# Kernel optimization log

Measured on AMD Instinct MI355X. Metric: run time of the kernel, lower is better.

## Reference

```python
import jax, jax.numpy as jnp
import numpy as np

HEADS = 8

def setup_inputs() -> dict:
    key = jax.random.key(0)
    ks = jax.random.split(key, 5)
    B, C, H, W = 2, 256, 64, 64
    dim = C
    x = jax.random.normal(ks[0], (B, C, H, W), dtype=jnp.float32)
    # Linear weights stored as [in, out] so y = x @ W + b
    w_qkv = jax.random.normal(ks[1], (dim, 3 * dim), dtype=jnp.float32) * (dim ** -0.5)
    b_qkv = jax.random.normal(ks[2], (3 * dim,), dtype=jnp.float32) * 0.02
    w_out = jax.random.normal(ks[3], (dim, dim), dtype=jnp.float32) * (dim ** -0.5)
    b_out = jax.random.normal(ks[4], (dim,), dtype=jnp.float32) * 0.02
    return {"x": x, "w_qkv": w_qkv, "b_qkv": b_qkv, "w_out": w_out, "b_out": b_out}

def reference(x, w_qkv, b_qkv, w_out, b_out):
    B, C, H, W = x.shape
    h = HEADS
    d = C // h
    scale = d ** -0.5
    # [B, C, H, W] -> [B, N, C]
    tokens = x.reshape(B, C, H * W).transpose(0, 2, 1)
    qkv = tokens @ w_qkv + b_qkv  # [B, N, 3C]
    q, k, v = jnp.split(qkv, 3, axis=-1)
    def to_heads(t):
        Bn, N, _ = t.shape
        return t.reshape(Bn, N, h, d).transpose(0, 2, 1, 3)  # [B, h, N, d]
    q, k, v = map(to_heads, (q, k, v))
    dots = jnp.einsum('bhnd,bhmd->bhnm', q, k) * scale  # [B, h, N, N]
    attn = jax.nn.softmax(dots, axis=-1)
    out = jnp.einsum('bhnm,bhmd->bhnd', attn, v)  # [B, h, N, d]
    out = out.transpose(0, 2, 1, 3).reshape(B, H * W, C)  # [B, N, C]
    out = out @ w_out + b_out
    return out.transpose(0, 2, 1).reshape(B, C, H, W)
```

## Files before the change

kernel.cpp:

```cpp
#include <hip/hip_runtime.h>

typedef __attribute__((ext_vector_type(8))) short s16x8;
typedef __attribute__((ext_vector_type(4))) float f32x4;
typedef __attribute__((ext_vector_type(16))) float f32x16;
typedef __attribute__((ext_vector_type(2))) unsigned u32x2;
typedef __attribute__((ext_vector_type(4))) unsigned u32x4;

#define MFMA32(a, b, c) __builtin_amdgcn_mfma_f32_16x16x32_bf16((a), (b), (c), 0, 0, 0)

#if __has_builtin(__builtin_amdgcn_mfma_f32_32x32x16_bf16)
#define MFMA3216(a, b, c) __builtin_amdgcn_mfma_f32_32x32x16_bf16((a), (b), (c), 0, 0, 0)
#else
#define MFMA3216(a, b, c) (c)
#endif

#if __has_builtin(__builtin_amdgcn_exp2f)
#define EXP2F(x) __builtin_amdgcn_exp2f(x)
#else
#define EXP2F(x) __exp2f(x)
#endif

#if __has_builtin(__builtin_amdgcn_rcpf)
#define RCPF(x) __builtin_amdgcn_rcpf(x)
#else
#define RCPF(x) (1.0f / (x))
#endif

#define SL2E 0.25507313f

__device__ __forceinline__ unsigned pkrne(float a, float b) {
  unsigned ua = __builtin_bit_cast(unsigned, a);
  unsigned ub = __builtin_bit_cast(unsigned, b);
  ua += 0x7FFFu + ((ua >> 16) & 1u);
  ub += 0x7FFFu + ((ub >> 16) & 1u);
  return __builtin_amdgcn_perm(ub, ua, 0x07060302u);
}

__device__ __forceinline__ unsigned pktrunc(float a, float b) {
  return __builtin_amdgcn_perm(__builtin_bit_cast(unsigned, b),
                               __builtin_bit_cast(unsigned, a), 0x07060302u);
}

__device__ __forceinline__ unsigned short bfr(float f) {
  unsigned u = __builtin_bit_cast(unsigned, f);
  u += 0x7FFFu + ((u >> 16) & 1u);
  return (unsigned short)(u >> 16);
}

__device__ __forceinline__ float bflo(unsigned u) {
  return __builtin_bit_cast(float, u << 16);
}
__device__ __forceinline__ float bfhi(unsigned u) {
  return __builtin_bit_cast(float, u & 0xFFFF0000u);
}

__device__ __forceinline__ u32x2 plswap(unsigned a, unsigned b) {
#if __has_builtin(__builtin_amdgcn_permlane32_swap)
  return __builtin_amdgcn_permlane32_swap(a, b, false, false);
#else
  unsigned sa = (unsigned)__shfl_xor((int)a, 32, 64);
  unsigned sb = (unsigned)__shfl_xor((int)b, 32, 64);
  bool hi = (threadIdx.x & 63) >= 32;
  u32x2 r;
  r.x = hi ? sb : a;
  r.y = hi ? b : sa;
  return r;
#endif
}

__global__ __launch_bounds__(256) void prep_kernel(
    const float* __restrict__ x, const float* __restrict__ wqkv,
    const float* __restrict__ wout, ushort* __restrict__ xbf,
    ushort* __restrict__ wT, ushort* __restrict__ woT) {
  const int t = threadIdx.x;
  const int sub = t & 15, grp = t >> 4;
  const int id = blockIdx.x;
  const float* src;
  ushort* dst;
  int src_ld, k0, n0;
  float sc = 1.f;
  if (id < 512) {
    int mt = id & 63, kt = (id >> 6) & 3, b = id >> 8;
    src = x + (size_t)b * 256 * 4096;
    src_ld = 4096;
    dst = xbf + (size_t)b * 4096 * 256;
    k0 = kt * 64;
    n0 = mt * 64;
  } else if (id < 560) {
    int r = id - 512, nt = r % 12, kt = r / 12;
    src = wqkv;
    src_ld = 768;
    dst = wT;
    k0 = kt * 64;
    n0 = nt * 64;
    if (n0 < 256) sc = SL2E;
  } else {
    int r = id - 560, nt = r & 3, kt = r >> 2;
    src = wout;
    src_ld = 256;
    dst = woT;
    k0 = kt * 64;
    n0 = nt * 64;
  }
  const int k = k0 + grp * 4;
  const int n = n0 + sub * 4;
  unsigned d0[4], d1[4];
#pragma unroll
  for (int i = 0; i < 4; ++i) {
    float4 v = *(const float4*)(src + (size_t)(k + i) * src_ld + n);
    d0[i] = pkrne(v.x * sc, v.y * sc);
    d1[i] = pkrne(v.z * sc, v.w * sc);
  }
  u32x2 r0 = {__builtin_amdgcn_perm(d0[1], d0[0], 0x05040100u),
              __builtin_amdgcn_perm(d0[3], d0[2], 0x05040100u)};
  u32x2 r1 = {__builtin_amdgcn_perm(d0[1], d0[0], 0x07060302u),
              __builtin_amdgcn_perm(d0[3], d0[2], 0x07060302u)};
  u32x2 r2 = {__builtin_amdgcn_perm(d1[1], d1[0], 0x05040100u),
              __builtin_amdgcn_perm(d1[3], d1[2], 0x05040100u)};
  u32x2 r3 = {__builtin_amdgcn_perm(d1[1], d1[0], 0x07060302u),
              __builtin_amdgcn_perm(d1[3], d1[2], 0x07060302u)};
  *(u32x2*)(dst + (size_t)(n + 0) * 256 + k) = r0;
  *(u32x2*)(dst + (size_t)(n + 1) * 256 + k) = r1;
  *(u32x2*)(dst + (size_t)(n + 2) * 256 + k) = r2;
  *(u32x2*)(dst + (size_t)(n + 3) * 256 + k) = r3;
}

__global__ __launch_bounds__(256) void qkv_kernel(
    const ushort* __restrict__ xbf, const ushort* __restrict__ wT,
    const float* __restrict__ bq, ushort* __restrict__ QG,
    ushort* __restrict__ KG, ushort* __restrict__ VtG) {
  __shared__ __align__(16) ushort Wl[64][40];
  __shared__ __align__(16) ushort Xl[128][40];
  const int t0 = blockIdx.x * 128;
  const int n0 = blockIdx.y * 64;
  const int t = threadIdx.x;
  const int wid = t >> 6, lane = t & 63;
  const int wy = wid >> 1, wx = wid & 1;
  const int quad = lane >> 4, l16 = lane & 15;
  f32x4 acc[2][4] = {};
  const int wr = t >> 2, wsg = t & 3;
  for (int k0 = 0; k0 < 256; k0 += 32) {
    __syncthreads();
    *(uint4*)&Wl[wr][wsg * 8] =
        *(const uint4*)(wT + (size_t)(n0 + wr) * 256 + k0 + wsg * 8);
#pragma unroll
    for (int i = 0; i < 2; ++i) {
      int fid = t + 256 * i, row = fid >> 2, seg = fid & 3;
      *(uint4*)&Xl[row][seg * 8] =
          *(const uint4*)(xbf + (size_t)(t0 + row) * 256 + k0 + seg * 8);
    }
    __syncthreads();
    s16x8 wf[2], xf[4];
#pragma unroll
    for (int i = 0; i < 2; ++i)
      wf[i] = *(const s16x8*)&Wl[32 * wy + 16 * i + l16][quad * 8];
#pragma unroll
    for (int j = 0; j < 4; ++j)
      xf[j] = *(const s16x8*)&Xl[64 * wx + 16 * j + l16][quad * 8];
#pragma unroll
    for (int i = 0; i < 2; ++i)
#pragma unroll
      for (int j = 0; j < 4; ++j) acc[i][j] = MFMA32(wf[i], xf[j], acc[i][j]);
  }
  if (n0 < 256) {
#pragma unroll
    for (int i = 0; i < 2; ++i) {
      int nb = n0 + 32 * wy + 16 * i + 4 * quad;
      float4 b4 = *(const float4*)(bq + nb);
      float bx0 = b4.x * SL2E, bx1 = b4.y * SL2E, bx2 = b4.z * SL2E,
            bx3 = b4.w * SL2E;
      int h = ((nb & 255) >> 5);
      int dd0 = nb & 31;
#pragma unroll
      for (int j = 0; j < 4; ++j) {
        int tok = t0 + 64 * wx + 16 * j + l16;
        int b = tok >> 12, tokn = tok & 4095;
        u32x2 pk = {pkrne(acc[i][j][0] + bx0, acc[i][j][1] + bx1),
                    pkrne(acc[i][j][2] + bx2, acc[i][j][3] + bx3)};
        *(u32x2*)(QG + ((size_t)(b * 8 + h) * 4096 + tokn) * 32 + dd0) = pk;
      }
    }
  } else if (n0 < 512) {
#pragma unroll
    for (int i = 0; i < 2; ++i) {
      int nb = n0 + 32 * wy + 16 * i + 4 * quad;
      float4 b4 = *(const float4*)(bq + nb);
      float bx0 = b4.x, bx1 = b4.y, bx2 = b4.z, bx3 = b4.w;
      int h = ((nb & 255) >> 5);
      size_t fo = (size_t)i * 512 + (quad >> 1) * 256 + (quad & 1) * 4;
#pragma unroll
      for (int j = 0; j < 4; ++j) {
        int tok = t0 + 64 * wx + 16 * j + l16;
        int b = tok >> 12, tokn = tok & 4095;
        int tl = tokn >> 6, ss = (tokn >> 5) & 1, l5 = tokn & 31;
        u32x2 pk = {pkrne(acc[i][j][0] + bx0, acc[i][j][1] + bx1),
                    pkrne(acc[i][j][2] + bx2, acc[i][j][3] + bx3)};
        *(u32x2*)(KG + (size_t)(b * 8 + h) * 131072 + (size_t)tl * 2048 +
                  ss * 1024 + l5 * 8 + fo) = pk;
      }
    }
  } else {
#pragma unroll
    for (int i = 0; i < 2; ++i) {
      int nb = n0 + 32 * wy + 16 * i + 4 * quad;
      float4 b4 = *(const float4*)(bq + nb);
      float bb[4] = {b4.x, b4.y, b4.z, b4.w};
#pragma unroll
      for (int r = 0; r < 4; ++r) {
        int nn = nb + r - 512;
        int h = nn >> 5, d = nn & 31;
#pragma unroll
        for (int j = 0; j < 4; ++j) {
          int tok = t0 + 64 * wx + 16 * j + l16;
          int b = tok >> 12, tokn = tok & 4095;
          int tl = tokn >> 6, ss = (tokn >> 5) & 1;
          int hV = (tokn >> 4) & 1, hii = (tokn >> 3) & 1, e = tokn & 7;
          VtG[(size_t)(b * 8 + h) * 131072 + (size_t)tl * 2048 + ss * 1024 +
              hV * 512 + hii * 256 + d * 8 + e] = bfr(acc[i][j][r] + bb[r]);
        }
      }
    }
  }
}

__global__ __launch_bounds__(256, 4) void attn_split(
    const ushort* __restrict__ QG, const ushort* __restrict__ KG,
    const ushort* __restrict__ VtG, ushort* __restrict__ OF0,
    ushort* __restrict__ OFb, float* __restrict__ LF) {
  const int id = blockIdx.x;
  const int bh = (id & 7) * 2 + ((id >> 3) & 1);
  const int q0 = ((id >> 4) & 31) * 128;
  const int sp = id >> 9;
  const int kt0 = sp * 32;
  const int niter = 32;
  const int t = threadIdx.x;
  const int wid = t >> 6, lane = t & 63;
  const int l5 = lane & 31, hi = lane >> 5;
  const ushort* qp = QG + (size_t)bh * 4096 * 32;
  const ushort* kgp = KG + (size_t)bh * 131072 + (size_t)kt0 * 2048;
  const ushort* vgp = VtG + (size_t)bh * 131072 + (size_t)kt0 * 2048;
  const int qw = q0 + 32 * wid;
  const ushort* qrow = qp + (size_t)(qw + l5) * 32 + hi * 8;
  const s16x8 qf0 = *(const s16x8*)(qrow);
  const s16x8 qf1 = *(const s16x8*)(qrow + 16);
  f32x16 o = {};
  f32x16 o_l = {};
  const s16x8 ones8 = {(short)0x3F80, (short)0x3F80, (short)0x3F80,
                       (short)0x3F80, (short)0x3F80, (short)0x3F80,
                       (short)0x3F80, (short)0x3F80};
  const int lo8 = lane * 8;
  for (int i = 0; i < niter; ++i) {
    const ushort* kt = kgp + (size_t)i * 2048;
    const ushort* vt = vgp + (size_t)i * 2048;
    s16x8 k00 = *(const s16x8*)(kt + lo8);
    s16x8 k01 = *(const s16x8*)(kt + 512 + lo8);
    s16x8 v00 = *(const s16x8*)(vt + lo8);
    s16x8 v01 = *(const s16x8*)(vt + 512 + lo8);
    s16x8 k10 = *(const s16x8*)(kt + 1024 + lo8);
    s16x8 k11 = *(const s16x8*)(kt + 1536 + lo8);
    s16x8 v10 = *(const s16x8*)(vt + 1024 + lo8);
    s16x8 v11 = *(const s16x8*)(vt + 1536 + lo8);
#pragma unroll
    for (int s = 0; s < 2; ++s) {
      const s16x8 ka0 = s ? k10 : k00;
      const s16x8 ka1 = s ? k11 : k01;
      const s16x8 va0 = s ? v10 : v00;
      const s16x8 va1 = s ? v11 : v01;
      f32x16 S = {};
      S = MFMA3216(ka0, qf0, S);
      S = MFMA3216(ka1, qf1, S);
      unsigned w8[8];
#pragma unroll
      for (int ii = 0; ii < 8; ++ii)
        w8[ii] = pktrunc(EXP2F(S[2 * ii]), EXP2F(S[2 * ii + 1]));
      u32x2 sw0 = plswap(w8[0], w8[2]);
      u32x2 sw1 = plswap(w8[1], w8[3]);
      u32x2 sw2 = plswap(w8[4], w8[6]);
      u32x2 sw3 = plswap(w8[5], w8[7]);
      u32x4 pa0 = {sw0.x, sw1.x, sw0.y, sw1.y};
      u32x4 pa1 = {sw2.x, sw3.x, sw2.y, sw3.y};
      const s16x8 pA0 = __builtin_bit_cast(s16x8, pa0);
      const s16x8 pA1 = __builtin_bit_cast(s16x8, pa1);
      o = MFMA3216(pA0, va0, o);
      o = MFMA3216(pA1, va1, o);
      o_l = MFMA3216(pA0, ones8, o_l);
      o_l = MFMA3216(pA1, ones8, o_l);
    }
  }
  ushort* OFs = (sp == 0) ? OF0 : OFb;
  float* LFs = LF + (size_t)sp * 65536;
#pragma unroll
  for (int r = 0; r < 16; ++r) {
    int q = qw + (r & 3) + 8 * (r >> 2) + 4 * hi;
    OFs[((size_t)bh * 4096 + q) * 32 + l5] = bfr(o[r]);
  }
  float lval = o_l[0];
#pragma unroll
  for (int r = 1; r < 16; ++r) lval = (l5 == r) ? o_l[r] : lval;
  if (l5 < 16)
    LFs[(size_t)bh * 4096 + qw + (l5 & 3) + 8 * (l5 >> 2) + 4 * hi] = lval;
}

__global__ __launch_bounds__(256) void proj_split(
    const ushort* __restrict__ OF0, const ushort* __restrict__ OFb,
    const float* __restrict__ LF, const ushort* __restrict__ woT,
    const float* __restrict__ bo, float* __restrict__ out) {
  __shared__ __align__(16) ushort Wl[64][40];
  __shared__ __align__(16) ushort Xl[128][40];
  const int t0 = blockIdx.x * 128;
  const int c0 = blockIdx.y * 64;
  const int t = threadIdx.x;
  const int wid = t >> 6, lane = t & 63;
  const int wy = wid >> 1, wx = wid & 1;
  const int quad = lane >> 4, l16 = lane & 15;
  f32x4 acc[2][4] = {};
  const int wr = t >> 2, wsg = t & 3;
  const int c8 = (t & 7) * 4;
  for (int k0 = 0; k0 < 256; k0 += 32) {
    __syncthreads();
    *(uint4*)&Wl[wr][wsg * 8] =
        *(const uint4*)(woT + (size_t)(c0 + wr) * 256 + k0 + wsg * 8);
    const int hh = k0 >> 5;
#pragma unroll
    for (int p = 0; p < 4; ++p) {
      int row = 32 * p + (t >> 3);
      int tok = t0 + row, bb = tok >> 12, tokn = tok & 4095;
      size_t ro = (size_t)(bb * 8 + hh) * 4096 + tokn;
      size_t oi = ro * 32 + c8;
      uint2 a0 = *(const uint2*)(OF0 + oi);
      uint2 a1 = *(const uint2*)(OFb + oi);
      float l = LF[ro] + LF[65536 + ro];
      float inv = RCPF(l);
      f32x4 s;
      s[0] = bflo(a0.x) + bflo(a1.x);
      s[1] = bfhi(a0.x) + bfhi(a1.x);
      s[2] = bflo(a0.y) + bflo(a1.y);
      s[3] = bfhi(a0.y) + bfhi(a1.y);
      s *= inv;
      u32x2 pk = {pkrne(s[0], s[1]), pkrne(s[2], s[3])};
      *(u32x2*)&Xl[row][c8] = pk;
    }
    __syncthreads();
    s16x8 wf[2], xf[4];
#pragma unroll
    for (int i = 0; i < 2; ++i)
      wf[i] = *(const s16x8*)&Wl[32 * wy + 16 * i + l16][quad * 8];
#pragma unroll
    for (int j = 0; j < 4; ++j)
      xf[j] = *(const s16x8*)&Xl[64 * wx + 16 * j + l16][quad * 8];
#pragma unroll
    for (int i = 0; i < 2; ++i)
#pragma unroll
      for (int j = 0; j < 4; ++j) acc[i][j] = MFMA32(wf[i], xf[j], acc[i][j]);
  }
#pragma unroll
  for (int i = 0; i < 2; ++i) {
    int cb = c0 + 32 * wy + 16 * i + 4 * quad;
    float4 b4 = *(const float4*)(bo + cb);
    float bb[4] = {b4.x, b4.y, b4.z, b4.w};
#pragma unroll
    for (int j = 0; j < 4; ++j) {
      int tok = t0 + 64 * wx + 16 * j + l16;
      int b = tok >> 12, tokn = tok & 4095;
#pragma unroll
      for (int r = 0; r < 4; ++r)
        out[((size_t)(b * 256 + cb + r)) * 4096 + tokn] = acc[i][j][r] + bb[r];
    }
  }
}

extern "C" void kernel_launch(void* const* d_in, const int* in_sizes, int n_in,
                              void* d_out, int out_size, void* d_ws, size_t ws_size,
                              hipStream_t stream) {
  (void)in_sizes; (void)n_in; (void)out_size; (void)ws_size;
  const float* x = (const float*)d_in[0];
  const float* wq = (const float*)d_in[1];
  const float* bq = (const float*)d_in[2];
  const float* wo = (const float*)d_in[3];
  const float* bo = (const float*)d_in[4];
  float* out = (float*)d_out;
  ushort* ws = (ushort*)d_ws;
  ushort* xbf = ws;
  ushort* OF0 = ws;
  ushort* QG  = ws + 2097152;
  ushort* KG  = ws + 4194304;
  ushort* VtG = ws + 6291456;
  ushort* wT  = ws + 8388608;
  ushort* woT = ws + 8585216;
  ushort* OFb = ws + 8650752;
  float* LF = (float*)(ws + 12845056);
  prep_kernel<<<576, 256, 0, stream>>>(x, wq, wo, xbf, wT, woT);
  qkv_kernel<<<dim3(64, 12), 256, 0, stream>>>(xbf, wT, bq, QG, KG, VtG);
  attn_split<<<1024, 256, 0, stream>>>(QG, KG, VtG, OF0, OFb, LF);
  proj_split<<<dim3(64, 4), 256, 0, stream>>>(OF0, OFb, LF, woT, bo, out);
}
```

Baseline: 143.4 us.

## Stage K/V tiles through triple-buffered LDS with async loads and software-pipelined softmax

The attention kernel now copies K and V tiles into a three-deep shared-memory ring using direct global-to-LDS loads, replacing the per-wave global reads. The score MFMAs for one half-tile are interleaved with the softmax and PV step of the previous half-tile, so memory latency and exp work can overlap with matrix math. The K/V tiles are shared across the four waves of a block, with one barrier per iteration. Separately, the output projection tile is halved to 64 tokens, which doubles the grid for better CU occupancy at the cost of more redundant weight loads.

```diff
diff --git a/kernel.cpp b/kernel.cpp
--- a/kernel.cpp
+++ b/kernel.cpp
@@ -65,6 +65,19 @@
   r.x = hi ? sb : a;
   r.y = hi ? b : sa;
   return r;
+#endif
+}
+
+__device__ __forceinline__ void stage16(const ushort* g, ushort* l, int lane) {
+#if __has_builtin(__builtin_amdgcn_global_load_lds)
+  __builtin_amdgcn_global_load_lds(
+      (__attribute__((address_space(1))) unsigned int*)(unsigned long long)(
+          const void*)g,
+      (__attribute__((address_space(3))) unsigned int*)(unsigned)(
+          unsigned long long)(const void*)l,
+      16, 0, 0);
+#else
+  *(uint4*)(l + lane * 8) = *(const uint4*)g;
 #endif
 }
 
@@ -223,10 +236,41 @@
   }
 }
 
+struct AttnAcc {
+  f32x16 o;
+  f32x16 o_l;
+};
+
+__device__ __forceinline__ void softpv(const f32x16& S, const ushort* vhalf,
+                                       int lane, f32x16& o, f32x16& o_l) {
+  const s16x8 ones8 = {(short)0x3F80, (short)0x3F80, (short)0x3F80,
+                       (short)0x3F80, (short)0x3F80, (short)0x3F80,
+                       (short)0x3F80, (short)0x3F80};
+  unsigned w8[8];
+#pragma unroll
+  for (int ii = 0; ii < 8; ++ii)
+    w8[ii] = pktrunc(EXP2F(S[2 * ii]), EXP2F(S[2 * ii + 1]));
+  u32x2 sw0 = plswap(w8[0], w8[2]);
+  u32x2 sw1 = plswap(w8[1], w8[3]);
+  u32x2 sw2 = plswap(w8[4], w8[6]);
+  u32x2 sw3 = plswap(w8[5], w8[7]);
+  u32x4 pa0 = {sw0.x, sw1.x, sw0.y, sw1.y};
+  u32x4 pa1 = {sw2.x, sw3.x, sw2.y, sw3.y};
+  const s16x8 pA0 = __builtin_bit_cast(s16x8, pa0);
+  const s16x8 pA1 = __builtin_bit_cast(s16x8, pa1);
+  const s16x8 va0 = *(const s16x8*)(vhalf + lane * 8);
+  const s16x8 va1 = *(const s16x8*)(vhalf + 512 + lane * 8);
+  o = MFMA3216(pA0, va0, o);
+  o = MFMA3216(pA1, va1, o);
+  o_l = MFMA3216(pA0, ones8, o_l);
+  o_l = MFMA3216(pA1, ones8, o_l);
+}
+
 __global__ __launch_bounds__(256, 4) void attn_split(
     const ushort* __restrict__ QG, const ushort* __restrict__ KG,
     const ushort* __restrict__ VtG, ushort* __restrict__ OF0,
     ushort* __restrict__ OFb, float* __restrict__ LF) {
+  __shared__ __align__(64) ushort KVs[3][4096];
   const int id = blockIdx.x;
   const int bh = (id & 7) * 2 + ((id >> 3) & 1);
   const int q0 = ((id >> 4) & 31) * 128;
@@ -243,50 +287,46 @@
   const ushort* qrow = qp + (size_t)(qw + l5) * 32 + hi * 8;
   const s16x8 qf0 = *(const s16x8*)(qrow);
   const s16x8 qf1 = *(const s16x8*)(qrow + 16);
+  const int kdst = wid * 512;
+  const ushort* kpre = kgp + kdst + lane * 8;
+  const ushort* vpre = vgp + kdst + lane * 8;
+  stage16(kpre, &KVs[0][kdst], lane);
+  stage16(vpre, &KVs[0][2048 + kdst], lane);
+  kpre += 2048;
+  vpre += 2048;
+  __syncthreads();
   f32x16 o = {};
   f32x16 o_l = {};
-  const s16x8 ones8 = {(short)0x3F80, (short)0x3F80, (short)0x3F80,
-                       (short)0x3F80, (short)0x3F80, (short)0x3F80,
-                       (short)0x3F80, (short)0x3F80};
+  f32x16 S1p = {};
+  int b = 0, bm1 = 2, bp1 = 1;
   const int lo8 = lane * 8;
   for (int i = 0; i < niter; ++i) {
-    const ushort* kt = kgp + (size_t)i * 2048;
-    const ushort* vt = vgp + (size_t)i * 2048;
-    s16x8 k00 = *(const s16x8*)(kt + lo8);
-    s16x8 k01 = *(const s16x8*)(kt + 512 + lo8);
-    s16x8 v00 = *(const s16x8*)(vt + lo8);
-    s16x8 v01 = *(const s16x8*)(vt + 512 + lo8);
-    s16x8 k10 = *(const s16x8*)(kt + 1024 + lo8);
-    s16x8 k11 = *(const s16x8*)(kt + 1536 + lo8);
-    s16x8 v10 = *(const s16x8*)(vt + 1024 + lo8);
-    s16x8 v11 = *(const s16x8*)(vt + 1536 + lo8);
-#pragma unroll
-    for (int s = 0; s < 2; ++s) {
-      const s16x8 ka0 = s ? k10 : k00;
-      const s16x8 ka1 = s ? k11 : k01;
-      const s16x8 va0 = s ? v10 : v00;
-      const s16x8 va1 = s ? v11 : v01;
-      f32x16 S = {};
-      S = MFMA3216(ka0, qf0, S);
-      S = MFMA3216(ka1, qf1, S);
-      unsigned w8[8];
-#pragma unroll
-      for (int ii = 0; ii < 8; ++ii)
-        w8[ii] = pktrunc(EXP2F(S[2 * ii]), EXP2F(S[2 * ii + 1]));
-      u32x2 sw0 = plswap(w8[0], w8[2]);
-      u32x2 sw1 = plswap(w8[1], w8[3]);
-      u32x2 sw2 = plswap(w8[4], w8[6]);
-      u32x2 sw3 = plswap(w8[5], w8[7]);
-      u32x4 pa0 = {sw0.x, sw1.x, sw0.y, sw1.y};
-      u32x4 pa1 = {sw2.x, sw3.x, sw2.y, sw3.y};
-      const s16x8 pA0 = __builtin_bit_cast(s16x8, pa0);
-      const s16x8 pA1 = __builtin_bit_cast(s16x8, pa1);
-      o = MFMA3216(pA0, va0, o);
-      o = MFMA3216(pA1, va1, o);
-      o_l = MFMA3216(pA0, ones8, o_l);
-      o_l = MFMA3216(pA1, ones8, o_l);
-    }
-  }
+    if (i + 1 < niter) {
+      stage16(kpre, &KVs[bp1][kdst], lane);
+      stage16(vpre, &KVs[bp1][2048 + kdst], lane);
+      kpre += 2048;
+      vpre += 2048;
+    }
+    const ushort* kb = &KVs[b][0];
+    const s16x8 ka00 = *(const s16x8*)(kb + lo8);
+    const s16x8 ka01 = *(const s16x8*)(kb + 512 + lo8);
+    f32x16 S0 = {};
+    S0 = MFMA3216(ka00, qf0, S0);
+    S0 = MFMA3216(ka01, qf1, S0);
+    if (i > 0) softpv(S1p, &KVs[bm1][2048 + 1024], lane, o, o_l);
+    const s16x8 ka10 = *(const s16x8*)(kb + 1024 + lo8);
+    const s16x8 ka11 = *(const s16x8*)(kb + 1536 + lo8);
+    f32x16 S1 = {};
+    S1 = MFMA3216(ka10, qf0, S1);
+    S1 = MFMA3216(ka11, qf1, S1);
+    softpv(S0, &KVs[b][2048], lane, o, o_l);
+    S1p = S1;
+    __syncthreads();
+    bm1 = b;
+    b = bp1;
+    bp1 = (bp1 + 1 == 3) ? 0 : bp1 + 1;
+  }
+  softpv(S1p, &KVs[bm1][2048 + 1024], lane, o, o_l);
   ushort* OFs = (sp == 0) ? OF0 : OFb;
   float* LFs = LF + (size_t)sp * 65536;
 #pragma unroll
@@ -306,14 +346,14 @@
     const float* __restrict__ LF, const ushort* __restrict__ woT,
     const float* __restrict__ bo, float* __restrict__ out) {
   __shared__ __align__(16) ushort Wl[64][40];
-  __shared__ __align__(16) ushort Xl[128][40];
-  const int t0 = blockIdx.x * 128;
+  __shared__ __align__(16) ushort Xl[64][40];
+  const int t0 = blockIdx.x * 64;
   const int c0 = blockIdx.y * 64;
   const int t = threadIdx.x;
   const int wid = t >> 6, lane = t & 63;
   const int wy = wid >> 1, wx = wid & 1;
   const int quad = lane >> 4, l16 = lane & 15;
-  f32x4 acc[2][4] = {};
+  f32x4 acc[2][2] = {};
   const int wr = t >> 2, wsg = t & 3;
   const int c8 = (t & 7) * 4;
   for (int k0 = 0; k0 < 256; k0 += 32) {
@@ -322,7 +362,7 @@
         *(const uint4*)(woT + (size_t)(c0 + wr) * 256 + k0 + wsg * 8);
     const int hh = k0 >> 5;
 #pragma unroll
-    for (int p = 0; p < 4; ++p) {
+    for (int p = 0; p < 2; ++p) {
       int row = 32 * p + (t >> 3);
       int tok = t0 + row, bb = tok >> 12, tokn = tok & 4095;
       size_t ro = (size_t)(bb * 8 + hh) * 4096 + tokn;
@@ -341,17 +381,17 @@
       *(u32x2*)&Xl[row][c8] = pk;
     }
     __syncthreads();
-    s16x8 wf[2], xf[4];
+    s16x8 wf[2], xf[2];
 #pragma unroll
     for (int i = 0; i < 2; ++i)
       wf[i] = *(const s16x8*)&Wl[32 * wy + 16 * i + l16][quad * 8];
 #pragma unroll
-    for (int j = 0; j < 4; ++j)
-      xf[j] = *(const s16x8*)&Xl[64 * wx + 16 * j + l16][quad * 8];
+    for (int j = 0; j < 2; ++j)
+      xf[j] = *(const s16x8*)&Xl[32 * wx + 16 * j + l16][quad * 8];
 #pragma unroll
     for (int i = 0; i < 2; ++i)
 #pragma unroll
-      for (int j = 0; j < 4; ++j) acc[i][j] = MFMA32(wf[i], xf[j], acc[i][j]);
+      for (int j = 0; j < 2; ++j) acc[i][j] = MFMA32(wf[i], xf[j], acc[i][j]);
   }
 #pragma unroll
   for (int i = 0; i < 2; ++i) {
@@ -359,8 +399,8 @@
     float4 b4 = *(const float4*)(bo + cb);
     float bb[4] = {b4.x, b4.y, b4.z, b4.w};
 #pragma unroll
-    for (int j = 0; j < 4; ++j) {
-      int tok = t0 + 64 * wx + 16 * j + l16;
+    for (int j = 0; j < 2; ++j) {
+      int tok = t0 + 32 * wx + 16 * j + l16;
       int b = tok >> 12, tokn = tok & 4095;
 #pragma unroll
       for (int r = 0; r < 4; ++r)
@@ -392,5 +432,5 @@
   prep_kernel<<<576, 256, 0, stream>>>(x, wq, wo, xbf, wT, woT);
   qkv_kernel<<<dim3(64, 12), 256, 0, stream>>>(xbf, wT, bq, QG, KG, VtG);
   attn_split<<<1024, 256, 0, stream>>>(QG, KG, VtG, OF0, OFb, LF);
-  proj_split<<<dim3(64, 4), 256, 0, stream>>>(OF0, OFb, LF, woT, bo, out);
-}
+  proj_split<<<dim3(128, 4), 256, 0, stream>>>(OF0, OFb, LF, woT, bo, out);
+}
```

Result: faster. 136.6 us (-4.7%).

## Split attention keys three ways, software-pipeline K/V loads, shrink projection tiles

Applied to the files above, without the earlier changes.

The attention kernel now splits the 64 key tiles across three partitions instead of two, giving 1536 blocks, with the occupancy hint lowered from 4 to 3. Its inner loop double-buffers K/V register loads so the next tile's loads overlap the current tile's MFMAs. The projection kernel sums three partial outputs and normalizers and uses 64-token tiles, launching twice as many blocks. The aim is better GPU fill and latency hiding, at the cost of more partial-result traffic and register pressure.

```diff
diff --git a/kernel.cpp b/kernel.cpp
--- a/kernel.cpp
+++ b/kernel.cpp
@@ -223,7 +223,48 @@
   }
 }
 
-__global__ __launch_bounds__(256, 4) void attn_split(
+__device__ __forceinline__ void softpv(const f32x16& S, s16x8 va0, s16x8 va1,
+                                       f32x16& o, f32x16& o_l) {
+  const s16x8 ones8 = {(short)0x3F80, (short)0x3F80, (short)0x3F80,
+                       (short)0x3F80, (short)0x3F80, (short)0x3F80,
+                       (short)0x3F80, (short)0x3F80};
+  unsigned w8[8];
+#pragma unroll
+  for (int ii = 0; ii < 8; ++ii)
+    w8[ii] = pktrunc(EXP2F(S[2 * ii]), EXP2F(S[2 * ii + 1]));
+  u32x2 sw0 = plswap(w8[0], w8[2]);
+  u32x2 sw1 = plswap(w8[1], w8[3]);
+  u32x2 sw2 = plswap(w8[4], w8[6]);
+  u32x2 sw3 = plswap(w8[5], w8[7]);
+  u32x4 pa0 = {sw0.x, sw1.x, sw0.y, sw1.y};
+  u32x4 pa1 = {sw2.x, sw3.x, sw2.y, sw3.y};
+  const s16x8 pA0 = __builtin_bit_cast(s16x8, pa0);
+  const s16x8 pA1 = __builtin_bit_cast(s16x8, pa1);
+  o = MFMA3216(pA0, va0, o);
+  o = MFMA3216(pA1, va1, o);
+  o_l = MFMA3216(pA0, ones8, o_l);
+  o_l = MFMA3216(pA1, ones8, o_l);
+}
+
+#define LDT(F0, F1, F2, F3, P)            \
+  {                                       \
+    F0 = *(const s16x8*)((P));            \
+    F1 = *(const s16x8*)((P) + 512);      \
+    F2 = *(const s16x8*)((P) + 1024);     \
+    F3 = *(const s16x8*)((P) + 1536);     \
+  }
+
+#define TILE(K0, K1, K2, K3, V0, V1, V2, V3)   \
+  {                                            \
+    f32x16 S0 = MFMA3216(K0, qf0, fz);         \
+    S0 = MFMA3216(K1, qf1, S0);                \
+    softpv(S0, V0, V1, o, o_l);                \
+    f32x16 S1 = MFMA3216(K2, qf0, fz);         \
+    S1 = MFMA3216(K3, qf1, S1);                \
+    softpv(S1, V2, V3, o, o_l);                \
+  }
+
+__global__ __launch_bounds__(256, 3) void attn_split(
     const ushort* __restrict__ QG, const ushort* __restrict__ KG,
     const ushort* __restrict__ VtG, ushort* __restrict__ OF0,
     ushort* __restrict__ OFb, float* __restrict__ LF) {
@@ -231,63 +272,47 @@
   const int bh = (id & 7) * 2 + ((id >> 3) & 1);
   const int q0 = ((id >> 4) & 31) * 128;
   const int sp = id >> 9;
-  const int kt0 = sp * 32;
-  const int niter = 32;
+  const int kt0 = (sp * 64 + 2) / 3;
+  const int niter = ((sp + 1) * 64 + 2) / 3 - kt0;
   const int t = threadIdx.x;
   const int wid = t >> 6, lane = t & 63;
   const int l5 = lane & 31, hi = lane >> 5;
   const ushort* qp = QG + (size_t)bh * 4096 * 32;
-  const ushort* kgp = KG + (size_t)bh * 131072 + (size_t)kt0 * 2048;
-  const ushort* vgp = VtG + (size_t)bh * 131072 + (size_t)kt0 * 2048;
+  const int lo8 = lane * 8;
+  const ushort* kn = KG + (size_t)bh * 131072 + (size_t)kt0 * 2048 + lo8;
+  const ushort* vn = VtG + (size_t)bh * 131072 + (size_t)kt0 * 2048 + lo8;
   const int qw = q0 + 32 * wid;
   const ushort* qrow = qp + (size_t)(qw + l5) * 32 + hi * 8;
   const s16x8 qf0 = *(const s16x8*)(qrow);
   const s16x8 qf1 = *(const s16x8*)(qrow + 16);
   f32x16 o = {};
   f32x16 o_l = {};
-  const s16x8 ones8 = {(short)0x3F80, (short)0x3F80, (short)0x3F80,
-                       (short)0x3F80, (short)0x3F80, (short)0x3F80,
-                       (short)0x3F80, (short)0x3F80};
-  const int lo8 = lane * 8;
-  for (int i = 0; i < niter; ++i) {
-    const ushort* kt = kgp + (size_t)i * 2048;
-    const ushort* vt = vgp + (size_t)i * 2048;
-    s16x8 k00 = *(const s16x8*)(kt + lo8);
-    s16x8 k01 = *(const s16x8*)(kt + 512 + lo8);
-    s16x8 v00 = *(const s16x8*)(vt + lo8);
-    s16x8 v01 = *(const s16x8*)(vt + 512 + lo8);
-    s16x8 k10 = *(const s16x8*)(kt + 1024 + lo8);
-    s16x8 k11 = *(const s16x8*)(kt + 1536 + lo8);
-    s16x8 v10 = *(const s16x8*)(vt + 1024 + lo8);
-    s16x8 v11 = *(const s16x8*)(vt + 1536 + lo8);
-#pragma unroll
-    for (int s = 0; s < 2; ++s) {
-      const s16x8 ka0 = s ? k10 : k00;
-      const s16x8 ka1 = s ? k11 : k01;
-      const s16x8 va0 = s ? v10 : v00;
-      const s16x8 va1 = s ? v11 : v01;
-      f32x16 S = {};
-      S = MFMA3216(ka0, qf0, S);
-      S = MFMA3216(ka1, qf1, S);
-      unsigned w8[8];
-#pragma unroll
-      for (int ii = 0; ii < 8; ++ii)
-        w8[ii] = pktrunc(EXP2F(S[2 * ii]), EXP2F(S[2 * ii + 1]));
-      u32x2 sw0 = plswap(w8[0], w8[2]);
-      u32x2 sw1 = plswap(w8[1], w8[3]);
-      u32x2 sw2 = plswap(w8[4], w8[6]);
-      u32x2 sw3 = plswap(w8[5], w8[7]);
-      u32x4 pa0 = {sw0.x, sw1.x, sw0.y, sw1.y};
-      u32x4 pa1 = {sw2.x, sw3.x, sw2.y, sw3.y};
-      const s16x8 pA0 = __builtin_bit_cast(s16x8, pa0);
-      const s16x8 pA1 = __builtin_bit_cast(s16x8, pa1);
-      o = MFMA3216(pA0, va0, o);
-      o = MFMA3216(pA1, va1, o);
-      o_l = MFMA3216(pA0, ones8, o_l);
-      o_l = MFMA3216(pA1, ones8, o_l);
-    }
-  }
-  ushort* OFs = (sp == 0) ? OF0 : OFb;
+  const f32x16 fz = {};
+  s16x8 KA0, KA1, KA2, KA3, VA0, VA1, VA2, VA3;
+  s16x8 KB0, KB1, KB2, KB3, VB0, VB1, VB2, VB3;
+  LDT(KA0, KA1, KA2, KA3, kn)
+  LDT(VA0, VA1, VA2, VA3, vn)
+  kn += 2048;
+  vn += 2048;
+  const int pairs = niter >> 1;
+  for (int p = 0; p < pairs; ++p) {
+    LDT(KB0, KB1, KB2, KB3, kn)
+    LDT(VB0, VB1, VB2, VB3, vn)
+    kn += 2048;
+    vn += 2048;
+    TILE(KA0, KA1, KA2, KA3, VA0, VA1, VA2, VA3)
+    if (2 * p + 2 < niter) {
+      LDT(KA0, KA1, KA2, KA3, kn)
+      LDT(VA0, VA1, VA2, VA3, vn)
+      kn += 2048;
+      vn += 2048;
+    }
+    TILE(KB0, KB1, KB2, KB3, VB0, VB1, VB2, VB3)
+  }
+  if (niter & 1) {
+    TILE(KA0, KA1, KA2, KA3, VA0, VA1, VA2, VA3)
+  }
+  ushort* OFs = (sp == 0) ? OF0 : OFb + (size_t)(sp - 1) * 2097152;
   float* LFs = LF + (size_t)sp * 65536;
 #pragma unroll
   for (int r = 0; r < 16; ++r) {
@@ -306,14 +331,14 @@
     const float* __restrict__ LF, const ushort* __restrict__ woT,
     const float* __restrict__ bo, float* __restrict__ out) {
   __shared__ __align__(16) ushort Wl[64][40];
-  __shared__ __align__(16) ushort Xl[128][40];
-  const int t0 = blockIdx.x * 128;
+  __shared__ __align__(16) ushort Xl[64][40];
+  const int t0 = blockIdx.x * 64;
   const int c0 = blockIdx.y * 64;
   const int t = threadIdx.x;
   const int wid = t >> 6, lane = t & 63;
   const int wy = wid >> 1, wx = wid & 1;
   const int quad = lane >> 4, l16 = lane & 15;
-  f32x4 acc[2][4] = {};
+  f32x4 acc[2][2] = {};
   const int wr = t >> 2, wsg = t & 3;
   const int c8 = (t & 7) * 4;
   for (int k0 = 0; k0 < 256; k0 += 32) {
@@ -322,36 +347,37 @@
         *(const uint4*)(woT + (size_t)(c0 + wr) * 256 + k0 + wsg * 8);
     const int hh = k0 >> 5;
 #pragma unroll
-    for (int p = 0; p < 4; ++p) {
+    for (int p = 0; p < 2; ++p) {
       int row = 32 * p + (t >> 3);
       int tok = t0 + row, bb = tok >> 12, tokn = tok & 4095;
       size_t ro = (size_t)(bb * 8 + hh) * 4096 + tokn;
       size_t oi = ro * 32 + c8;
       uint2 a0 = *(const uint2*)(OF0 + oi);
       uint2 a1 = *(const uint2*)(OFb + oi);
-      float l = LF[ro] + LF[65536 + ro];
+      uint2 a2 = *(const uint2*)(OFb + 2097152 + oi);
+      float l = LF[ro] + LF[65536 + ro] + LF[131072 + ro];
       float inv = RCPF(l);
       f32x4 s;
-      s[0] = bflo(a0.x) + bflo(a1.x);
-      s[1] = bfhi(a0.x) + bfhi(a1.x);
-      s[2] = bflo(a0.y) + bflo(a1.y);
-      s[3] = bfhi(a0.y) + bfhi(a1.y);
+      s[0] = bflo(a0.x) + bflo(a1.x) + bflo(a2.x);
+      s[1] = bfhi(a0.x) + bfhi(a1.x) + bfhi(a2.x);
+      s[2] = bflo(a0.y) + bflo(a1.y) + bflo(a2.y);
+      s[3] = bfhi(a0.y) + bfhi(a1.y) + bfhi(a2.y);
       s *= inv;
       u32x2 pk = {pkrne(s[0], s[1]), pkrne(s[2], s[3])};
       *(u32x2*)&Xl[row][c8] = pk;
     }
     __syncthreads();
-    s16x8 wf[2], xf[4];
+    s16x8 wf[2], xf[2];
 #pragma unroll
     for (int i = 0; i < 2; ++i)
       wf[i] = *(const s16x8*)&Wl[32 * wy + 16 * i + l16][quad * 8];
 #pragma unroll
-    for (int j = 0; j < 4; ++j)
-      xf[j] = *(const s16x8*)&Xl[64 * wx + 16 * j + l16][quad * 8];
+    for (int j = 0; j < 2; ++j)
+      xf[j] = *(const s16x8*)&Xl[32 * wx + 16 * j + l16][quad * 8];
 #pragma unroll
     for (int i = 0; i < 2; ++i)
 #pragma unroll
-      for (int j = 0; j < 4; ++j) acc[i][j] = MFMA32(wf[i], xf[j], acc[i][j]);
+      for (int j = 0; j < 2; ++j) acc[i][j] = MFMA32(wf[i], xf[j], acc[i][j]);
   }
 #pragma unroll
   for (int i = 0; i < 2; ++i) {
@@ -359,8 +385,8 @@
     float4 b4 = *(const float4*)(bo + cb);
     float bb[4] = {b4.x, b4.y, b4.z, b4.w};
 #pragma unroll
-    for (int j = 0; j < 4; ++j) {
-      int tok = t0 + 64 * wx + 16 * j + l16;
+    for (int j = 0; j < 2; ++j) {
+      int tok = t0 + 32 * wx + 16 * j + l16;
       int b = tok >> 12, tokn = tok & 4095;
 #pragma unroll
       for (int r = 0; r < 4; ++r)
@@ -391,6 +417,6 @@
   float* LF = (float*)(ws + 12845056);
   prep_kernel<<<576, 256, 0, stream>>>(x, wq, wo, xbf, wT, woT);
   qkv_kernel<<<dim3(64, 12), 256, 0, stream>>>(xbf, wT, bq, QG, KG, VtG);
-  attn_split<<<1024, 256, 0, stream>>>(QG, KG, VtG, OF0, OFb, LF);
-  proj_split<<<dim3(64, 4), 256, 0, stream>>>(OF0, OFb, LF, woT, bo, out);
-}
+  attn_split<<<1536, 256, 0, stream>>>(QG, KG, VtG, OF0, OFb, LF);
+  proj_split<<<dim3(128, 4), 256, 0, stream>>>(OF0, OFb, LF, woT, bo, out);
+}
```

New measurement: 139.6 us. 1.03x faster.
